# Kernel tuning notes

Hardware: AMD Instinct MI355X
Metric: run time of the kernel (lower is better)

Reference implementation:

```python
import jax, jax.numpy as jnp
import numpy as np

N_NODES = 100000
N_EDGES = 300000
D = 128
HID = 128

def setup_inputs() -> dict:
    key = jax.random.key(0)
    ks = jax.random.split(key, 12)
    s = lambda fan_in: 1.0 / np.sqrt(fan_in)
    return {
        "user_emb": jax.random.normal(ks[0], (N_NODES, D), jnp.float32),
        "item_emb": jax.random.normal(ks[1], (N_NODES, D), jnp.float32),
        "ei_ui": jax.random.randint(ks[2], (2, N_EDGES), 0, N_NODES, jnp.int64),
        "ei_iu": jax.random.randint(ks[3], (2, N_EDGES), 0, N_NODES, jnp.int64),
        "W_bi_ui": jax.random.normal(ks[4], (2 * D, HID), jnp.float32) * s(2 * D),
        "b_bi_ui": jnp.zeros((HID,), jnp.float32),
        "W1_ui": jax.random.normal(ks[5], (HID, HID), jnp.float32) * s(HID),
        "b1_ui": jnp.zeros((HID,), jnp.float32),
        "W2_ui": jax.random.normal(ks[6], (HID, 1), jnp.float32) * s(HID),
        "b2_ui": jnp.zeros((1,), jnp.float32),
        "W_bi_iu": jax.random.normal(ks[7], (2 * D, HID), jnp.float32) * s(2 * D),
        "b_bi_iu": jnp.zeros((HID,), jnp.float32),
        "W1_iu": jax.random.normal(ks[8], (HID, HID), jnp.float32) * s(HID),
        "b1_iu": jnp.zeros((HID,), jnp.float32),
        "W2_iu": jax.random.normal(ks[9], (HID, 1), jnp.float32) * s(HID),
        "b2_iu": jnp.zeros((1,), jnp.float32),
    }

def _decode_edge_type(src_emb, dst_emb, edge_index, W_bi, b_bi, W1, b1, W2, b2):
    # gather endpoint embeddings and concat -> [E, 2D]
    e = jnp.concatenate([src_emb[edge_index[0]], dst_emb[edge_index[1]]], axis=1)
    h = jax.nn.elu(e @ W_bi + b_bi)          # bilinear -> ELU
    h = jax.nn.elu(h @ W1 + b1)              # linear1 -> ELU
    p = jax.nn.sigmoid(h @ W2 + b2)          # linear2 -> sigmoid
    return p.reshape(-1)                     # [E]

def reference(user_emb, item_emb, ei_ui, ei_iu,
              W_bi_ui, b_bi_ui, W1_ui, b1_ui, W2_ui, b2_ui,
              W_bi_iu, b_bi_iu, W1_iu, b1_iu, W2_iu, b2_iu):
    # edge type (user, clicks, item): source=user, target=item
    p_ui = _decode_edge_type(user_emb, item_emb, ei_ui,
                             W_bi_ui, b_bi_ui, W1_ui, b1_ui, W2_ui, b2_ui)
    # edge type (item, clicked_by, user): source=item, target=user
    p_iu = _decode_edge_type(item_emb, user_emb, ei_iu,
                             W_bi_iu, b_bi_iu, W1_iu, b1_iu, W2_iu, b2_iu)
    return jnp.stack([p_ui, p_iu])  # [2, E]
```

## Files before the change

kernel.cpp:

```cpp
#include <hip/hip_runtime.h>

typedef __attribute__((ext_vector_type(8))) short short8;
typedef __attribute__((ext_vector_type(4))) float float4v;
typedef __attribute__((ext_vector_type(4))) int int4v;

#define E_EDGES 300000
#define EPB 128
#define NBLK ((E_EDGES + EPB - 1) / EPB)
#define TAB_ELEMS 12800000

__device__ __forceinline__ short f2bf(float f) {
    unsigned u = __float_as_uint(f);
    return (short)((u + 0x7FFFu + ((u >> 16) & 1u)) >> 16);
}
__device__ __forceinline__ unsigned pk_bf16(float a, float b) {
    unsigned ua = __float_as_uint(a), ub = __float_as_uint(b);
    ua += 0x7FFFu + ((ua >> 16) & 1u);
    ub += 0x7FFFu + ((ub >> 16) & 1u);
    return __builtin_amdgcn_perm(ub, ua, 0x07060302);
}
__device__ __forceinline__ void cp16(const void* g, void* l) {
    __builtin_amdgcn_global_load_lds(
        (const __attribute__((address_space(1))) unsigned int*)g,
        (__attribute__((address_space(3))) unsigned int*)l, 16, 0, 0);
}

__global__ void prep_all(const float* __restrict__ ue, const float* __restrict__ ie,
                         const float* __restrict__ Wbi_ui, const float* __restrict__ W1_ui,
                         const float* __restrict__ Wbi_iu, const float* __restrict__ W1_iu,
                         short* __restrict__ ws) {
    __shared__ short tr[64 * 68];
    const int t = blockIdx.y;
    const int tid = threadIdx.x;
    if (blockIdx.x < 1024) {
        const float* src = t ? ie : ue;
        short* dst = ws + 98304 + (size_t)t * TAB_ELEMS;
        const int stride = 1024 * 256;
        for (int g = blockIdx.x * 256 + tid; g < TAB_ELEMS / 8; g += stride) {
            const float* p = src + (size_t)g * 8;
            float4v v0 = ((const float4v*)p)[0];
            float4v v1 = ((const float4v*)p)[1];
            int4v w = { (int)pk_bf16(v0[0], v0[1]), (int)pk_bf16(v0[2], v0[3]),
                        (int)pk_bf16(v1[0], v1[1]), (int)pk_bf16(v1[2], v1[3]) };
            *(int4v*)(dst + (size_t)g * 8) = w;
        }
        return;
    }
    const int m = blockIdx.x - 1024;
    const float* W; int k0, n0, obase;
    if (m < 8) {
        int kt = m >> 1, nh = m & 1;
        W = t ? Wbi_iu : Wbi_ui; k0 = kt * 64; n0 = nh * 64;
        obase = t * 32768 + kt * 8192;
    } else {
        int mm = m - 8; int kt = mm >> 1, nh = mm & 1;
        W = t ? W1_iu : W1_ui; k0 = kt * 64; n0 = nh * 64;
        obase = 65536 + t * 16384 + kt * 8192;
    }
    for (int it = 0; it < 16; ++it) {
        int flat = it * 256 + tid;
        int kk = flat >> 6, nn = flat & 63;
        tr[nn * 68 + kk] = f2bf(W[(size_t)(k0 + kk) * 128 + n0 + nn]);
    }
    __syncthreads();
    for (int it = 0; it < 16; ++it) {
        int flat = it * 256 + tid;
        int nn = flat >> 6, kk = flat & 63;
        int n = n0 + nn;
        ws[obase + n * 64 + (kk ^ ((n & 7) << 3))] = tr[nn * 68 + kk];
    }
}

template<bool BF16G>
__launch_bounds__(256, 4)
__global__ void edge_decoder(
    const float* __restrict__ user_emb, const float* __restrict__ item_emb,
    const int* __restrict__ ei_ui, const int* __restrict__ ei_iu,
    const float* __restrict__ b_bi_ui, const float* __restrict__ b1_ui,
    const float* __restrict__ W2_ui, const float* __restrict__ b2_ui,
    const float* __restrict__ b_bi_iu, const float* __restrict__ b1_iu,
    const float* __restrict__ W2_iu, const float* __restrict__ b2_iu,
    const short* __restrict__ ws, const short* __restrict__ tab,
    float* __restrict__ out)
{
    __shared__ short Blds[2][128 * 64];

    const int type = blockIdx.y;
    const int e0 = blockIdx.x * EPB;
    const int tid = threadIdx.x;
    const int wave = tid >> 6, lane = tid & 63;
    const int q = lane >> 4, ln = lane & 15;

    const int*   ei   = type ? ei_iu : ei_ui;
    const float* bbi  = type ? b_bi_iu : b_bi_ui;
    const float* b1v  = type ? b1_iu : b1_ui;
    const float* W2v  = type ? W2_iu : W2_ui;
    const float* b2v  = type ? b2_iu : b2_ui;
    const short* WbiT = ws + type * 32768;
    const short* W1T  = ws + 65536 + type * 16384;

    for (int c = 0; c < 4; ++c)
        cp16(WbiT + c * 2048 + tid * 8, &Blds[0][c * 2048 + tid * 8]);

    int si[2], di[2];
    for (int mt = 0; mt < 2; ++mt) {
        int erow = e0 + wave * 32 + mt * 16 + ln;
        int safe = (erow < E_EDGES) ? erow : 0;
        si[mt] = ei[safe];
        di[mt] = ei[E_EDGES + safe];
    }

    short8 a[2][8];
    if (BF16G) {
        for (int mt = 0; mt < 2; ++mt) {
            const short* sp = tab + (size_t)(type ? TAB_ELEMS : 0) + (size_t)si[mt] * 128;
            const short* dp = tab + (size_t)(type ? 0 : TAB_ELEMS) + (size_t)di[mt] * 128;
            for (int ks = 0; ks < 4; ++ks)
                a[mt][ks] = *(const short8*)(sp + ks * 32 + q * 8);
            for (int ks = 4; ks < 8; ++ks)
                a[mt][ks] = *(const short8*)(dp + (ks - 4) * 32 + q * 8);
        }
    } else {
        const float* srcT = type ? item_emb : user_emb;
        const float* dstT = type ? user_emb : item_emb;
        for (int mt = 0; mt < 2; ++mt)
            for (int ks = 0; ks < 8; ++ks) {
                const float* p = (ks < 4) ? (srcT + (size_t)si[mt] * 128 + ks * 32 + q * 8)
                                          : (dstT + (size_t)di[mt] * 128 + (ks - 4) * 32 + q * 8);
                float4v v0 = ((const float4v*)p)[0];
                float4v v1 = ((const float4v*)p)[1];
                int4v w = { (int)pk_bf16(v0[0], v0[1]), (int)pk_bf16(v0[2], v0[3]),
                            (int)pk_bf16(v1[0], v1[1]), (int)pk_bf16(v1[2], v1[3]) };
                a[mt][ks] = *(short8*)&w;
            }
    }

    float4v acc[2][8];
    for (int nt = 0; nt < 8; ++nt) {
        float bb = bbi[nt * 16 + ln];
        acc[0][nt] = (float4v){bb, bb, bb, bb};
        acc[1][nt] = acc[0][nt];
    }

    const int swz = (ln & 7) << 3;

    int cur = 0;
    for (int kt = 0; kt < 4; ++kt) {
        __syncthreads();
        const short* nxt = (kt < 3) ? (WbiT + (kt + 1) * 8192) : W1T;
        for (int c = 0; c < 4; ++c)
            cp16(nxt + c * 2048 + tid * 8, &Blds[cur ^ 1][c * 2048 + tid * 8]);
        __builtin_amdgcn_s_setprio(1);
        for (int ks2 = 0; ks2 < 2; ++ks2) {
            int ka = (ks2 * 32 + q * 8) ^ swz;
            int ks = kt * 2 + ks2;
            for (int nt = 0; nt < 8; ++nt) {
                short8 bf = *(const short8*)&Blds[cur][(nt * 16 + ln) * 64 + ka];
                acc[0][nt] = __builtin_amdgcn_mfma_f32_16x16x32_bf16(a[0][ks], bf, acc[0][nt], 0, 0, 0);
                acc[1][nt] = __builtin_amdgcn_mfma_f32_16x16x32_bf16(a[1][ks], bf, acc[1][nt], 0, 0, 0);
            }
        }
        __builtin_amdgcn_s_setprio(0);
        cur ^= 1;
    }

    __syncthreads();

    short* Hw = &Blds[cur ^ 1][wave * 2048];
    short8 a2[2][4];
    for (int mt = 0; mt < 2; ++mt) {
        for (int nt = 0; nt < 8; ++nt) {
            float4v v = acc[mt][nt];
            for (int r = 0; r < 4; ++r) {
                float x = v[r];
                float h = x > 0.f ? x : (__expf(x) - 1.f);
                int row = q * 4 + r;
                int g = (nt * 2 + (ln >> 3)) ^ (row & 7);
                Hw[row * 128 + g * 8 + (ln & 7)] = f2bf(h);
            }
        }
        for (int ks = 0; ks < 4; ++ks)
            a2[mt][ks] = *(const short8*)&Hw[ln * 128 + (((ks * 4 + q) ^ (ln & 7)) << 3)];
    }

    for (int nt = 0; nt < 8; ++nt) {
        float bb = b1v[nt * 16 + ln];
        acc[0][nt] = (float4v){bb, bb, bb, bb};
        acc[1][nt] = acc[0][nt];
    }

    __syncthreads();
    for (int c = 0; c < 4; ++c)
        cp16(W1T + 8192 + c * 2048 + tid * 8, &Blds[cur ^ 1][c * 2048 + tid * 8]);

    for (int kt = 0; kt < 2; ++kt) {
        if (kt == 1) __syncthreads();
        __builtin_amdgcn_s_setprio(1);
        for (int ks2 = 0; ks2 < 2; ++ks2) {
            int ka = (ks2 * 32 + q * 8) ^ swz;
            int ks = kt * 2 + ks2;
            for (int nt = 0; nt < 8; ++nt) {
                short8 bf = *(const short8*)&Blds[cur][(nt * 16 + ln) * 64 + ka];
                acc[0][nt] = __builtin_amdgcn_mfma_f32_16x16x32_bf16(a2[0][ks], bf, acc[0][nt], 0, 0, 0);
                acc[1][nt] = __builtin_amdgcn_mfma_f32_16x16x32_bf16(a2[1][ks], bf, acc[1][nt], 0, 0, 0);
            }
        }
        __builtin_amdgcn_s_setprio(0);
        cur ^= 1;
    }

    for (int mt = 0; mt < 2; ++mt) {
        float s0 = 0.f, s1 = 0.f, s2 = 0.f, s3 = 0.f;
        for (int nt = 0; nt < 8; ++nt) {
            float wv = W2v[nt * 16 + ln];
            float4v v = acc[mt][nt];
            float x;
            x = v[0]; x = x > 0.f ? x : (__expf(x) - 1.f); s0 += x * wv;
            x = v[1]; x = x > 0.f ? x : (__expf(x) - 1.f); s1 += x * wv;
            x = v[2]; x = x > 0.f ? x : (__expf(x) - 1.f); s2 += x * wv;
            x = v[3]; x = x > 0.f ? x : (__expf(x) - 1.f); s3 += x * wv;
        }
        for (int off = 1; off < 16; off <<= 1) {
            s0 += __shfl_xor(s0, off);
            s1 += __shfl_xor(s1, off);
            s2 += __shfl_xor(s2, off);
            s3 += __shfl_xor(s3, off);
        }
        if (ln < 4) {
            float sv = (ln == 0) ? s0 : (ln == 1) ? s1 : (ln == 2) ? s2 : s3;
            int e = e0 + wave * 32 + mt * 16 + q * 4 + ln;
            if (e < E_EDGES) {
                float z = sv + b2v[0];
                out[type * E_EDGES + e] = 1.f / (1.f + __expf(-z));
            }
        }
    }
}

extern "C" void kernel_launch(void* const* d_in, const int* in_sizes, int n_in,
                              void* d_out, int out_size, void* d_ws, size_t ws_size,
                              hipStream_t stream) {
    const float* user_emb = (const float*)d_in[0];
    const float* item_emb = (const float*)d_in[1];
    const int*   ei_ui    = (const int*)d_in[2];
    const int*   ei_iu    = (const int*)d_in[3];
    const float* W_bi_ui  = (const float*)d_in[4];
    const float* b_bi_ui  = (const float*)d_in[5];
    const float* W1_ui    = (const float*)d_in[6];
    const float* b1_ui    = (const float*)d_in[7];
    const float* W2_ui    = (const float*)d_in[8];
    const float* b2_ui    = (const float*)d_in[9];
    const float* W_bi_iu  = (const float*)d_in[10];
    const float* b_bi_iu  = (const float*)d_in[11];
    const float* W1_iu    = (const float*)d_in[12];
    const float* b1_iu    = (const float*)d_in[13];
    const float* W2_iu    = (const float*)d_in[14];
    const float* b2_iu    = (const float*)d_in[15];
    short* ws  = (short*)d_ws;
    short* tab = ws + 98304;
    float* out = (float*)d_out;

    const size_t need = 98304u * 2u + (size_t)2 * TAB_ELEMS * 2u;

    if (ws_size >= need) {
        hipLaunchKernelGGL(prep_all, dim3(1036, 2), dim3(256), 0, stream,
                           user_emb, item_emb, W_bi_ui, W1_ui, W_bi_iu, W1_iu, ws);
        edge_decoder<true><<<dim3(NBLK, 2), dim3(256), 0, stream>>>(
            user_emb, item_emb, ei_ui, ei_iu,
            b_bi_ui, b1_ui, W2_ui, b2_ui,
            b_bi_iu, b1_iu, W2_iu, b2_iu,
            ws, tab, out);
    } else {
        hipLaunchKernelGGL(prep_all, dim3(1036, 2), dim3(256), 0, stream,
                           user_emb, item_emb, W_bi_ui, W1_ui, W_bi_iu, W1_iu, ws);
        edge_decoder<false><<<dim3(NBLK, 2), dim3(256), 0, stream>>>(
            user_emb, item_emb, ei_ui, ei_iu,
            b_bi_ui, b1_ui, W2_ui, b2_ui,
            b_bi_iu, b1_iu, W2_iu, b2_iu,
            ws, tab, out);
    }
}
```

Measured before the change: 261.1 us.

## Interleave embedding gathers with layer-1 MFMA tiles to cut register use

Before this change, each thread gathered all 8 A-operand fragments (source and destination embeddings) ahead of the first GEMM. Now it keeps only two double-buffered halves and issues the destination-half loads between K-tiles, so gather latency overlaps with MFMA work. The register footprint for A fragments halves, which may help occupancy. The loops are also fully unrolled with constant buffer indices. The risk is that the gathers, now issued late, stall the later tiles if they do not arrive in time.

```diff
diff --git a/kernel.cpp b/kernel.cpp
--- a/kernel.cpp
+++ b/kernel.cpp
@@ -99,10 +99,12 @@
     const short* WbiT = ws + type * 32768;
     const short* W1T  = ws + 65536 + type * 16384;
 
+    #pragma unroll
     for (int c = 0; c < 4; ++c)
         cp16(WbiT + c * 2048 + tid * 8, &Blds[0][c * 2048 + tid * 8]);
 
     int si[2], di[2];
+    #pragma unroll
     for (int mt = 0; mt < 2; ++mt) {
         int erow = e0 + wave * 32 + mt * 16 + ln;
         int safe = (erow < E_EDGES) ? erow : 0;
@@ -110,32 +112,49 @@
         di[mt] = ei[E_EDGES + safe];
     }
 
-    short8 a[2][8];
+    const short* sp[2]; const short* dp[2];
+    const float* spf[2]; const float* dpf[2];
     if (BF16G) {
+        #pragma unroll
         for (int mt = 0; mt < 2; ++mt) {
-            const short* sp = tab + (size_t)(type ? TAB_ELEMS : 0) + (size_t)si[mt] * 128;
-            const short* dp = tab + (size_t)(type ? 0 : TAB_ELEMS) + (size_t)di[mt] * 128;
-            for (int ks = 0; ks < 4; ++ks)
-                a[mt][ks] = *(const short8*)(sp + ks * 32 + q * 8);
-            for (int ks = 4; ks < 8; ++ks)
-                a[mt][ks] = *(const short8*)(dp + (ks - 4) * 32 + q * 8);
+            sp[mt] = tab + (size_t)(type ? TAB_ELEMS : 0) + (size_t)si[mt] * 128 + q * 8;
+            dp[mt] = tab + (size_t)(type ? 0 : TAB_ELEMS) + (size_t)di[mt] * 128 + q * 8;
         }
     } else {
         const float* srcT = type ? item_emb : user_emb;
         const float* dstT = type ? user_emb : item_emb;
-        for (int mt = 0; mt < 2; ++mt)
-            for (int ks = 0; ks < 8; ++ks) {
-                const float* p = (ks < 4) ? (srcT + (size_t)si[mt] * 128 + ks * 32 + q * 8)
-                                          : (dstT + (size_t)di[mt] * 128 + (ks - 4) * 32 + q * 8);
-                float4v v0 = ((const float4v*)p)[0];
-                float4v v1 = ((const float4v*)p)[1];
-                int4v w = { (int)pk_bf16(v0[0], v0[1]), (int)pk_bf16(v0[2], v0[3]),
-                            (int)pk_bf16(v1[0], v1[1]), (int)pk_bf16(v1[2], v1[3]) };
-                a[mt][ks] = *(short8*)&w;
-            }
-    }
+        #pragma unroll
+        for (int mt = 0; mt < 2; ++mt) {
+            spf[mt] = srcT + (size_t)si[mt] * 128 + q * 8;
+            dpf[mt] = dstT + (size_t)di[mt] * 128 + q * 8;
+        }
+    }
+
+    short8 aA[2][2], aB[2][2];
+
+#define GATHER(BUF, HALF, OFF) do { \
+    _Pragma("unroll") \
+    for (int mt = 0; mt < 2; ++mt) { \
+        _Pragma("unroll") \
+        for (int k2 = 0; k2 < 2; ++k2) { \
+            if (BF16G) { \
+                BUF[mt][k2] = *(const short8*)((HALF ? dp[mt] : sp[mt]) + OFF + k2 * 32); \
+            } else { \
+                const float* p = (HALF ? dpf[mt] : spf[mt]) + OFF + k2 * 32; \
+                float4v v0 = ((const float4v*)p)[0]; \
+                float4v v1 = ((const float4v*)p)[1]; \
+                int4v w = { (int)pk_bf16(v0[0], v0[1]), (int)pk_bf16(v0[2], v0[3]), \
+                            (int)pk_bf16(v1[0], v1[1]), (int)pk_bf16(v1[2], v1[3]) }; \
+                BUF[mt][k2] = *(short8*)&w; \
+            } \
+        } \
+    } } while (0)
+
+    GATHER(aA, 0, 0);
+    GATHER(aB, 0, 64);
 
     float4v acc[2][8];
+    #pragma unroll
     for (int nt = 0; nt < 8; ++nt) {
         float bb = bbi[nt * 16 + ln];
         acc[0][nt] = (float4v){bb, bb, bb, bb};
@@ -144,33 +163,43 @@
 
     const int swz = (ln & 7) << 3;
 
-    int cur = 0;
-    for (int kt = 0; kt < 4; ++kt) {
-        __syncthreads();
-        const short* nxt = (kt < 3) ? (WbiT + (kt + 1) * 8192) : W1T;
-        for (int c = 0; c < 4; ++c)
-            cp16(nxt + c * 2048 + tid * 8, &Blds[cur ^ 1][c * 2048 + tid * 8]);
-        __builtin_amdgcn_s_setprio(1);
-        for (int ks2 = 0; ks2 < 2; ++ks2) {
-            int ka = (ks2 * 32 + q * 8) ^ swz;
-            int ks = kt * 2 + ks2;
-            for (int nt = 0; nt < 8; ++nt) {
-                short8 bf = *(const short8*)&Blds[cur][(nt * 16 + ln) * 64 + ka];
-                acc[0][nt] = __builtin_amdgcn_mfma_f32_16x16x32_bf16(a[0][ks], bf, acc[0][nt], 0, 0, 0);
-                acc[1][nt] = __builtin_amdgcn_mfma_f32_16x16x32_bf16(a[1][ks], bf, acc[1][nt], 0, 0, 0);
-            }
-        }
-        __builtin_amdgcn_s_setprio(0);
-        cur ^= 1;
-    }
+#define L1_TILE(KT, ABUF) do { \
+    __syncthreads(); \
+    const short* nxt = (KT < 3) ? (WbiT + (KT + 1) * 8192) : W1T; \
+    _Pragma("unroll") \
+    for (int c = 0; c < 4; ++c) \
+        cp16(nxt + c * 2048 + tid * 8, &Blds[(KT + 1) & 1][c * 2048 + tid * 8]); \
+    __builtin_amdgcn_s_setprio(1); \
+    _Pragma("unroll") \
+    for (int ks2 = 0; ks2 < 2; ++ks2) { \
+        int ka = (ks2 * 32 + q * 8) ^ swz; \
+        _Pragma("unroll") \
+        for (int nt = 0; nt < 8; ++nt) { \
+            short8 bf = *(const short8*)&Blds[KT & 1][(nt * 16 + ln) * 64 + ka]; \
+            acc[0][nt] = __builtin_amdgcn_mfma_f32_16x16x32_bf16(ABUF[0][ks2], bf, acc[0][nt], 0, 0, 0); \
+            acc[1][nt] = __builtin_amdgcn_mfma_f32_16x16x32_bf16(ABUF[1][ks2], bf, acc[1][nt], 0, 0, 0); \
+        } \
+    } \
+    __builtin_amdgcn_s_setprio(0); \
+    } while (0)
+
+    L1_TILE(0, aA);
+    GATHER(aA, 1, 0);
+    L1_TILE(1, aB);
+    GATHER(aB, 1, 64);
+    L1_TILE(2, aA);
+    L1_TILE(3, aB);
 
     __syncthreads();
 
-    short* Hw = &Blds[cur ^ 1][wave * 2048];
+    short* Hw = &Blds[1][wave * 2048];
     short8 a2[2][4];
+    #pragma unroll
     for (int mt = 0; mt < 2; ++mt) {
+        #pragma unroll
         for (int nt = 0; nt < 8; ++nt) {
             float4v v = acc[mt][nt];
+            #pragma unroll
             for (int r = 0; r < 4; ++r) {
                 float x = v[r];
                 float h = x > 0.f ? x : (__expf(x) - 1.f);
@@ -179,10 +208,12 @@
                 Hw[row * 128 + g * 8 + (ln & 7)] = f2bf(h);
             }
         }
+        #pragma unroll
         for (int ks = 0; ks < 4; ++ks)
             a2[mt][ks] = *(const short8*)&Hw[ln * 128 + (((ks * 4 + q) ^ (ln & 7)) << 3)];
     }
 
+    #pragma unroll
     for (int nt = 0; nt < 8; ++nt) {
         float bb = b1v[nt * 16 + ln];
         acc[0][nt] = (float4v){bb, bb, bb, bb};
@@ -190,27 +221,33 @@
     }
 
     __syncthreads();
+    #pragma unroll
     for (int c = 0; c < 4; ++c)
-        cp16(W1T + 8192 + c * 2048 + tid * 8, &Blds[cur ^ 1][c * 2048 + tid * 8]);
-
-    for (int kt = 0; kt < 2; ++kt) {
-        if (kt == 1) __syncthreads();
-        __builtin_amdgcn_s_setprio(1);
-        for (int ks2 = 0; ks2 < 2; ++ks2) {
-            int ka = (ks2 * 32 + q * 8) ^ swz;
-            int ks = kt * 2 + ks2;
-            for (int nt = 0; nt < 8; ++nt) {
-                short8 bf = *(const short8*)&Blds[cur][(nt * 16 + ln) * 64 + ka];
-                acc[0][nt] = __builtin_amdgcn_mfma_f32_16x16x32_bf16(a2[0][ks], bf, acc[0][nt], 0, 0, 0);
-                acc[1][nt] = __builtin_amdgcn_mfma_f32_16x16x32_bf16(a2[1][ks], bf, acc[1][nt], 0, 0, 0);
-            }
-        }
-        __builtin_amdgcn_s_setprio(0);
-        cur ^= 1;
-    }
-
+        cp16(W1T + 8192 + c * 2048 + tid * 8, &Blds[1][c * 2048 + tid * 8]);
+
+#define L2_TILE(KT) do { \
+    if (KT == 1) __syncthreads(); \
+    __builtin_amdgcn_s_setprio(1); \
+    _Pragma("unroll") \
+    for (int ks2 = 0; ks2 < 2; ++ks2) { \
+        int ka = (ks2 * 32 + q * 8) ^ swz; \
+        _Pragma("unroll") \
+        for (int nt = 0; nt < 8; ++nt) { \
+            short8 bf = *(const short8*)&Blds[KT][(nt * 16 + ln) * 64 + ka]; \
+            acc[0][nt] = __builtin_amdgcn_mfma_f32_16x16x32_bf16(a2[0][KT * 2 + ks2], bf, acc[0][nt], 0, 0, 0); \
+            acc[1][nt] = __builtin_amdgcn_mfma_f32_16x16x32_bf16(a2[1][KT * 2 + ks2], bf, acc[1][nt], 0, 0, 0); \
+        } \
+    } \
+    __builtin_amdgcn_s_setprio(0); \
+    } while (0)
+
+    L2_TILE(0);
+    L2_TILE(1);
+
+    #pragma unroll
     for (int mt = 0; mt < 2; ++mt) {
         float s0 = 0.f, s1 = 0.f, s2 = 0.f, s3 = 0.f;
+        #pragma unroll
         for (int nt = 0; nt < 8; ++nt) {
             float wv = W2v[nt * 16 + ln];
             float4v v = acc[mt][nt];
@@ -235,6 +272,9 @@
             }
         }
     }
+#undef GATHER
+#undef L1_TILE
+#undef L2_TILE
 }
 
 extern "C" void kernel_launch(void* const* d_in, const int* in_sizes, int n_in,
```

New measurement: 237.4 us. 9.1% less time.

## Make edge decoder persistent with resident weights and prefetched gathers

Applied to the files above, without the earlier changes.

Replaces the one-block-per-128-edges launch with a persistent grid of 128x2 blocks of 1024 threads. Each wave loops over 32-edge tiles. All bilinear and linear1 weights (96KB) are loaded into LDS once per block instead of being streamed and double-buffered per tile. The next tile's embedding gather and index load are issued right after the first GEMM so they overlap the rest of the computation, and the per-block barriers are removed. The costs are higher register pressure from holding two tiles of A fragments, 128KB of LDS per block (one block per CU), and fewer total waves to hide gather latency.

```diff
diff --git a/kernel.cpp b/kernel.cpp
--- a/kernel.cpp
+++ b/kernel.cpp
@@ -5,9 +5,10 @@
 typedef __attribute__((ext_vector_type(4))) int int4v;
 
 #define E_EDGES 300000
-#define EPB 128
-#define NBLK ((E_EDGES + EPB - 1) / EPB)
 #define TAB_ELEMS 12800000
+#define NTILES 9375
+#define DBLK 128
+#define NWAVESTOT (DBLK * 16)
 
 __device__ __forceinline__ short f2bf(float f) {
     unsigned u = __float_as_uint(f);
@@ -72,7 +73,7 @@
 }
 
 template<bool BF16G>
-__launch_bounds__(256, 4)
+__launch_bounds__(1024)
 __global__ void edge_decoder(
     const float* __restrict__ user_emb, const float* __restrict__ item_emb,
     const int* __restrict__ ei_ui, const int* __restrict__ ei_iu,
@@ -83,10 +84,10 @@
     const short* __restrict__ ws, const short* __restrict__ tab,
     float* __restrict__ out)
 {
-    __shared__ short Blds[2][128 * 64];
+    __shared__ short WL[6 * 8192];
+    __shared__ short HL[16 * 1024];
 
     const int type = blockIdx.y;
-    const int e0 = blockIdx.x * EPB;
     const int tid = threadIdx.x;
     const int wave = tid >> 6, lane = tid & 63;
     const int q = lane >> 4, ln = lane & 15;
@@ -98,143 +99,179 @@
     const float* b2v  = type ? b2_iu : b2_ui;
     const short* WbiT = ws + type * 32768;
     const short* W1T  = ws + 65536 + type * 16384;
-
-    for (int c = 0; c < 4; ++c)
-        cp16(WbiT + c * 2048 + tid * 8, &Blds[0][c * 2048 + tid * 8]);
-
-    int si[2], di[2];
-    for (int mt = 0; mt < 2; ++mt) {
-        int erow = e0 + wave * 32 + mt * 16 + ln;
-        int safe = (erow < E_EDGES) ? erow : 0;
-        si[mt] = ei[safe];
-        di[mt] = ei[E_EDGES + safe];
-    }
-
+    const short* tabS = tab + (size_t)(type ? TAB_ELEMS : 0);
+    const short* tabD = tab + (size_t)(type ? 0 : TAB_ELEMS);
+    const float* srcT = type ? item_emb : user_emb;
+    const float* dstT = type ? user_emb : item_emb;
+
+    #pragma unroll
+    for (int c = 0; c < 6; ++c) {
+        const short* src = (c < 4) ? (WbiT + c * 8192) : (W1T + (c - 4) * 8192);
+        cp16(src + tid * 8, &WL[c * 8192 + tid * 8]);
+    }
+
+    float bb0[8], bb1[8], w2r[8];
+    #pragma unroll
+    for (int nt = 0; nt < 8; ++nt) {
+        bb0[nt] = bbi[nt * 16 + ln];
+        bb1[nt] = b1v[nt * 16 + ln];
+        w2r[nt] = W2v[nt * 16 + ln];
+    }
+    const float b2s = b2v[0];
+
+    __syncthreads();
+
+    const int swz = (ln & 7) << 3;
+    const int t0 = blockIdx.x * 16 + wave;
+    short* Hw = &HL[wave * 1024];
+
+    int siN[2], diN[2];
     short8 a[2][8];
-    if (BF16G) {
+
+#define LOADIDX(T) do { \
+    int tt = (T) < NTILES ? (T) : 0; \
+    _Pragma("unroll") \
+    for (int mt = 0; mt < 2; ++mt) { \
+        int e = tt * 32 + mt * 16 + ln; \
+        siN[mt] = ei[e]; diN[mt] = ei[E_EDGES + e]; \
+    } } while (0)
+
+#define GATHER_A() do { \
+    if (BF16G) { \
+        _Pragma("unroll") \
+        for (int mt = 0; mt < 2; ++mt) { \
+            const short* sp = tabS + (size_t)siN[mt] * 128 + q * 8; \
+            const short* dp = tabD + (size_t)diN[mt] * 128 + q * 8; \
+            _Pragma("unroll") \
+            for (int ks = 0; ks < 4; ++ks) a[mt][ks] = *(const short8*)(sp + ks * 32); \
+            _Pragma("unroll") \
+            for (int ks = 0; ks < 4; ++ks) a[mt][4 + ks] = *(const short8*)(dp + ks * 32); \
+        } \
+    } else { \
+        _Pragma("unroll") \
+        for (int mt = 0; mt < 2; ++mt) { \
+            const float* sp = srcT + (size_t)siN[mt] * 128 + q * 8; \
+            const float* dp = dstT + (size_t)diN[mt] * 128 + q * 8; \
+            _Pragma("unroll") \
+            for (int ks = 0; ks < 8; ++ks) { \
+                const float* p = (ks < 4) ? (sp + ks * 32) : (dp + (ks - 4) * 32); \
+                float4v v0 = ((const float4v*)p)[0]; \
+                float4v v1 = ((const float4v*)p)[1]; \
+                int4v wv = { (int)pk_bf16(v0[0], v0[1]), (int)pk_bf16(v0[2], v0[3]), \
+                             (int)pk_bf16(v1[0], v1[1]), (int)pk_bf16(v1[2], v1[3]) }; \
+                a[mt][ks] = *(short8*)&wv; \
+            } \
+        } \
+    } } while (0)
+
+    LOADIDX(t0);
+    GATHER_A();
+    LOADIDX(t0 + NWAVESTOT);
+
+    for (int t = t0; t < NTILES; t += NWAVESTOT) {
+        float4v acc[2][8];
+        #pragma unroll
+        for (int nt = 0; nt < 8; ++nt) {
+            acc[0][nt] = (float4v){bb0[nt], bb0[nt], bb0[nt], bb0[nt]};
+            acc[1][nt] = acc[0][nt];
+        }
+
+        __builtin_amdgcn_s_setprio(1);
+        #pragma unroll
+        for (int kt = 0; kt < 4; ++kt) {
+            #pragma unroll
+            for (int ks2 = 0; ks2 < 2; ++ks2) {
+                const int ka = (ks2 * 32 + q * 8) ^ swz;
+                #pragma unroll
+                for (int nt = 0; nt < 8; ++nt) {
+                    short8 bf = *(const short8*)&WL[kt * 8192 + (nt * 16 + ln) * 64 + ka];
+                    acc[0][nt] = __builtin_amdgcn_mfma_f32_16x16x32_bf16(a[0][kt * 2 + ks2], bf, acc[0][nt], 0, 0, 0);
+                    acc[1][nt] = __builtin_amdgcn_mfma_f32_16x16x32_bf16(a[1][kt * 2 + ks2], bf, acc[1][nt], 0, 0, 0);
+                }
+            }
+        }
+        __builtin_amdgcn_s_setprio(0);
+
+        GATHER_A();
+        LOADIDX(t + 2 * NWAVESTOT);
+
+        short8 a2[2][4];
+        #pragma unroll
         for (int mt = 0; mt < 2; ++mt) {
-            const short* sp = tab + (size_t)(type ? TAB_ELEMS : 0) + (size_t)si[mt] * 128;
-            const short* dp = tab + (size_t)(type ? 0 : TAB_ELEMS) + (size_t)di[mt] * 128;
-            for (int ks = 0; ks < 4; ++ks)
-                a[mt][ks] = *(const short8*)(sp + ks * 32 + q * 8);
-            for (int ks = 4; ks < 8; ++ks)
-                a[mt][ks] = *(const short8*)(dp + (ks - 4) * 32 + q * 8);
-        }
-    } else {
-        const float* srcT = type ? item_emb : user_emb;
-        const float* dstT = type ? user_emb : item_emb;
-        for (int mt = 0; mt < 2; ++mt)
-            for (int ks = 0; ks < 8; ++ks) {
-                const float* p = (ks < 4) ? (srcT + (size_t)si[mt] * 128 + ks * 32 + q * 8)
-                                          : (dstT + (size_t)di[mt] * 128 + (ks - 4) * 32 + q * 8);
-                float4v v0 = ((const float4v*)p)[0];
-                float4v v1 = ((const float4v*)p)[1];
-                int4v w = { (int)pk_bf16(v0[0], v0[1]), (int)pk_bf16(v0[2], v0[3]),
-                            (int)pk_bf16(v1[0], v1[1]), (int)pk_bf16(v1[2], v1[3]) };
-                a[mt][ks] = *(short8*)&w;
-            }
-    }
-
-    float4v acc[2][8];
-    for (int nt = 0; nt < 8; ++nt) {
-        float bb = bbi[nt * 16 + ln];
-        acc[0][nt] = (float4v){bb, bb, bb, bb};
-        acc[1][nt] = acc[0][nt];
-    }
-
-    const int swz = (ln & 7) << 3;
-
-    int cur = 0;
-    for (int kt = 0; kt < 4; ++kt) {
-        __syncthreads();
-        const short* nxt = (kt < 3) ? (WbiT + (kt + 1) * 8192) : W1T;
-        for (int c = 0; c < 4; ++c)
-            cp16(nxt + c * 2048 + tid * 8, &Blds[cur ^ 1][c * 2048 + tid * 8]);
+            #pragma unroll
+            for (int h = 0; h < 2; ++h) {
+                #pragma unroll
+                for (int nt2 = 0; nt2 < 4; ++nt2) {
+                    float4v v = acc[mt][h * 4 + nt2];
+                    #pragma unroll
+                    for (int r = 0; r < 4; ++r) {
+                        float x = v[r];
+                        float hh = x > 0.f ? x : (__expf(x) - 1.f);
+                        int row = q * 4 + r;
+                        int g = (nt2 * 2 + (ln >> 3)) ^ (row & 7);
+                        Hw[row * 64 + g * 8 + (ln & 7)] = f2bf(hh);
+                    }
+                }
+                #pragma unroll
+                for (int ks2 = 0; ks2 < 2; ++ks2) {
+                    int g = (ks2 * 4 + q) ^ (ln & 7);
+                    a2[mt][h * 2 + ks2] = *(const short8*)&Hw[ln * 64 + g * 8];
+                }
+            }
+        }
+
+        #pragma unroll
+        for (int nt = 0; nt < 8; ++nt) {
+            acc[0][nt] = (float4v){bb1[nt], bb1[nt], bb1[nt], bb1[nt]};
+            acc[1][nt] = acc[0][nt];
+        }
+
         __builtin_amdgcn_s_setprio(1);
-        for (int ks2 = 0; ks2 < 2; ++ks2) {
-            int ka = (ks2 * 32 + q * 8) ^ swz;
-            int ks = kt * 2 + ks2;
+        #pragma unroll
+        for (int kt = 0; kt < 2; ++kt) {
+            #pragma unroll
+            for (int ks2 = 0; ks2 < 2; ++ks2) {
+                const int ka = (ks2 * 32 + q * 8) ^ swz;
+                #pragma unroll
+                for (int nt = 0; nt < 8; ++nt) {
+                    short8 bf = *(const short8*)&WL[(4 + kt) * 8192 + (nt * 16 + ln) * 64 + ka];
+                    acc[0][nt] = __builtin_amdgcn_mfma_f32_16x16x32_bf16(a2[0][kt * 2 + ks2], bf, acc[0][nt], 0, 0, 0);
+                    acc[1][nt] = __builtin_amdgcn_mfma_f32_16x16x32_bf16(a2[1][kt * 2 + ks2], bf, acc[1][nt], 0, 0, 0);
+                }
+            }
+        }
+        __builtin_amdgcn_s_setprio(0);
+
+        #pragma unroll
+        for (int mt = 0; mt < 2; ++mt) {
+            float s0 = 0.f, s1 = 0.f, s2 = 0.f, s3 = 0.f;
+            #pragma unroll
             for (int nt = 0; nt < 8; ++nt) {
-                short8 bf = *(const short8*)&Blds[cur][(nt * 16 + ln) * 64 + ka];
-                acc[0][nt] = __builtin_amdgcn_mfma_f32_16x16x32_bf16(a[0][ks], bf, acc[0][nt], 0, 0, 0);
-                acc[1][nt] = __builtin_amdgcn_mfma_f32_16x16x32_bf16(a[1][ks], bf, acc[1][nt], 0, 0, 0);
-            }
-        }
-        __builtin_amdgcn_s_setprio(0);
-        cur ^= 1;
-    }
-
-    __syncthreads();
-
-    short* Hw = &Blds[cur ^ 1][wave * 2048];
-    short8 a2[2][4];
-    for (int mt = 0; mt < 2; ++mt) {
-        for (int nt = 0; nt < 8; ++nt) {
-            float4v v = acc[mt][nt];
-            for (int r = 0; r < 4; ++r) {
-                float x = v[r];
-                float h = x > 0.f ? x : (__expf(x) - 1.f);
-                int row = q * 4 + r;
-                int g = (nt * 2 + (ln >> 3)) ^ (row & 7);
-                Hw[row * 128 + g * 8 + (ln & 7)] = f2bf(h);
-            }
-        }
-        for (int ks = 0; ks < 4; ++ks)
-            a2[mt][ks] = *(const short8*)&Hw[ln * 128 + (((ks * 4 + q) ^ (ln & 7)) << 3)];
-    }
-
-    for (int nt = 0; nt < 8; ++nt) {
-        float bb = b1v[nt * 16 + ln];
-        acc[0][nt] = (float4v){bb, bb, bb, bb};
-        acc[1][nt] = acc[0][nt];
-    }
-
-    __syncthreads();
-    for (int c = 0; c < 4; ++c)
-        cp16(W1T + 8192 + c * 2048 + tid * 8, &Blds[cur ^ 1][c * 2048 + tid * 8]);
-
-    for (int kt = 0; kt < 2; ++kt) {
-        if (kt == 1) __syncthreads();
-        __builtin_amdgcn_s_setprio(1);
-        for (int ks2 = 0; ks2 < 2; ++ks2) {
-            int ka = (ks2 * 32 + q * 8) ^ swz;
-            int ks = kt * 2 + ks2;
-            for (int nt = 0; nt < 8; ++nt) {
-                short8 bf = *(const short8*)&Blds[cur][(nt * 16 + ln) * 64 + ka];
-                acc[0][nt] = __builtin_amdgcn_mfma_f32_16x16x32_bf16(a2[0][ks], bf, acc[0][nt], 0, 0, 0);
-                acc[1][nt] = __builtin_amdgcn_mfma_f32_16x16x32_bf16(a2[1][ks], bf, acc[1][nt], 0, 0, 0);
-            }
-        }
-        __builtin_amdgcn_s_setprio(0);
-        cur ^= 1;
-    }
-
-    for (int mt = 0; mt < 2; ++mt) {
-        float s0 = 0.f, s1 = 0.f, s2 = 0.f, s3 = 0.f;
-        for (int nt = 0; nt < 8; ++nt) {
-            float wv = W2v[nt * 16 + ln];
-            float4v v = acc[mt][nt];
-            float x;
-            x = v[0]; x = x > 0.f ? x : (__expf(x) - 1.f); s0 += x * wv;
-            x = v[1]; x = x > 0.f ? x : (__expf(x) - 1.f); s1 += x * wv;
-            x = v[2]; x = x > 0.f ? x : (__expf(x) - 1.f); s2 += x * wv;
-            x = v[3]; x = x > 0.f ? x : (__expf(x) - 1.f); s3 += x * wv;
-        }
-        for (int off = 1; off < 16; off <<= 1) {
-            s0 += __shfl_xor(s0, off);
-            s1 += __shfl_xor(s1, off);
-            s2 += __shfl_xor(s2, off);
-            s3 += __shfl_xor(s3, off);
-        }
-        if (ln < 4) {
-            float sv = (ln == 0) ? s0 : (ln == 1) ? s1 : (ln == 2) ? s2 : s3;
-            int e = e0 + wave * 32 + mt * 16 + q * 4 + ln;
-            if (e < E_EDGES) {
-                float z = sv + b2v[0];
+                float wv = w2r[nt];
+                float4v v = acc[mt][nt];
+                float x;
+                x = v[0]; x = x > 0.f ? x : (__expf(x) - 1.f); s0 += x * wv;
+                x = v[1]; x = x > 0.f ? x : (__expf(x) - 1.f); s1 += x * wv;
+                x = v[2]; x = x > 0.f ? x : (__expf(x) - 1.f); s2 += x * wv;
+                x = v[3]; x = x > 0.f ? x : (__expf(x) - 1.f); s3 += x * wv;
+            }
+            #pragma unroll
+            for (int off = 1; off < 16; off <<= 1) {
+                s0 += __shfl_xor(s0, off);
+                s1 += __shfl_xor(s1, off);
+                s2 += __shfl_xor(s2, off);
+                s3 += __shfl_xor(s3, off);
+            }
+            if (ln < 4) {
+                float sv = (ln == 0) ? s0 : (ln == 1) ? s1 : (ln == 2) ? s2 : s3;
+                int e = t * 32 + mt * 16 + q * 4 + ln;
+                float z = sv + b2s;
                 out[type * E_EDGES + e] = 1.f / (1.f + __expf(-z));
             }
         }
     }
+#undef LOADIDX
+#undef GATHER_A
 }
 
 extern "C" void kernel_launch(void* const* d_in, const int* in_sizes, int n_in,
@@ -262,18 +299,16 @@
 
     const size_t need = 98304u * 2u + (size_t)2 * TAB_ELEMS * 2u;
 
+    hipLaunchKernelGGL(prep_all, dim3(1036, 2), dim3(256), 0, stream,
+                       user_emb, item_emb, W_bi_ui, W1_ui, W_bi_iu, W1_iu, ws);
     if (ws_size >= need) {
-        hipLaunchKernelGGL(prep_all, dim3(1036, 2), dim3(256), 0, stream,
-                           user_emb, item_emb, W_bi_ui, W1_ui, W_bi_iu, W1_iu, ws);
-        edge_decoder<true><<<dim3(NBLK, 2), dim3(256), 0, stream>>>(
+        edge_decoder<true><<<dim3(DBLK, 2), dim3(1024), 0, stream>>>(
             user_emb, item_emb, ei_ui, ei_iu,
             b_bi_ui, b1_ui, W2_ui, b2_ui,
             b_bi_iu, b1_iu, W2_iu, b2_iu,
             ws, tab, out);
     } else {
-        hipLaunchKernelGGL(prep_all, dim3(1036, 2), dim3(256), 0, stream,
-                           user_emb, item_emb, W_bi_ui, W1_ui, W_bi_iu, W1_iu, ws);
-        edge_decoder<false><<<dim3(NBLK, 2), dim3(256), 0, stream>>>(
+        edge_decoder<false><<<dim3(DBLK, 2), dim3(1024), 0, stream>>>(
             user_emb, item_emb, ei_ui, ei_iu,
             b_bi_ui, b1_ui, W2_ui, b2_ui,
             b_bi_iu, b1_iu, W2_iu, b2_iu,
```

Measured after the change: 430.2 us. +64.8%, slower.
